# Performance work log

Measured on AMD Instinct MI355X. Metric: run time of the kernel, lower is better.

The kernel has to match this reference:

```python
import jax, jax.numpy as jnp
import numpy as np

N, E, D = 10000, 160000, 512


def setup_inputs() -> dict:
    key = jax.random.key(0)
    ks = jax.random.split(key, 5)
    x = jax.random.normal(ks[0], (N, D), dtype=jnp.float32)
    edge_index = jax.random.randint(ks[1], (2, E), 0, N, dtype=jnp.int32)
    W = jax.random.normal(ks[2], (D, D), dtype=jnp.float32) * (1.0 / np.sqrt(D))
    a_src = jax.random.normal(ks[3], (D,), dtype=jnp.float32) * 0.1
    a_dst = jax.random.normal(ks[4], (D,), dtype=jnp.float32) * 0.1
    bias = jnp.zeros((D,), dtype=jnp.float32)
    return {"x": x, "edge_index": edge_index, "W": W,
            "a_src": a_src, "a_dst": a_dst, "bias": bias}


def reference(x, edge_index, W, a_src, a_dst, bias):
    n = x.shape[0]
    # PyG GATConv default: add self-loops
    loops = jnp.arange(n, dtype=edge_index.dtype)
    src = jnp.concatenate([edge_index[0], loops])  # [E+N]
    dst = jnp.concatenate([edge_index[1], loops])  # [E+N]

    h = x @ W.T                                    # [N, D] linear projection
    e_src = h @ a_src                              # [N]
    e_dst = h @ a_dst                              # [N]
    e = e_src[src] + e_dst[dst]                    # [E+N]
    neg_slope = 0.2
    e = jnp.where(e > 0, e, neg_slope * e)         # leaky_relu

    # per-destination softmax (stable); self-loops guarantee non-empty segments
    m = jax.ops.segment_max(e, dst, num_segments=n)
    e = jnp.exp(e - m[dst])
    s = jax.ops.segment_sum(e, dst, num_segments=n)
    alpha = e / s[dst]                             # [E+N]

    msg = alpha[:, None] * h[src]                  # [E+N, D]
    out = jax.ops.segment_sum(msg, dst, num_segments=n) + bias  # [N, D]

    # module forward: x + elu(gat(x, edge_index))
    return x + jax.nn.elu(out)
```

## Files before the change

kernel.cpp:

```cpp
#include <hip/hip_runtime.h>
#include <hip/hip_bf16.h>

using bf16x8 = __attribute__((ext_vector_type(8))) __bf16;
using f32x4  = __attribute__((ext_vector_type(4))) float;

#define DFEAT 512
#define SLOTS 64

static __device__ __forceinline__ unsigned short f2bfbits(float f) {
    union { float f; unsigned int u; } v; v.f = f;
    unsigned int u = v.u;
    unsigned int r = (u + 0x7fffu + ((u >> 16) & 1u)) >> 16;
    return (unsigned short)r;
}

static __device__ __forceinline__ bf16x8 cvt8(float4 lo, float4 hi) {
    union { __hip_bfloat162 h2[4]; bf16x8 v; } u;
    u.h2[0] = __float22bfloat162_rn(make_float2(lo.x, lo.y));
    u.h2[1] = __float22bfloat162_rn(make_float2(lo.z, lo.w));
    u.h2[2] = __float22bfloat162_rn(make_float2(hi.x, hi.y));
    u.h2[3] = __float22bfloat162_rn(make_float2(hi.z, hi.w));
    return u.v;
}

__global__ __launch_bounds__(256, 2) void gemm_h_kernel(
    const float* __restrict__ X, const float* __restrict__ Wm,
    const int* __restrict__ srcv, const int* __restrict__ dstv,
    const float* __restrict__ avs, const float* __restrict__ avd,
    unsigned short* __restrict__ H, float* __restrict__ es, float* __restrict__ ed,
    int* __restrict__ cur, int* __restrict__ slot,
    int N, int E, int nBlocks)
{
    __shared__ unsigned short Bl[64 * 512];

    {
        int T = E + N;
        int stride = nBlocks * 256;
        for (int i = blockIdx.x * 256 + threadIdx.x; i < T; i += stride) {
            int s, d;
            if (i < E) { s = srcv[i]; d = dstv[i]; }
            else       { s = d = i - E; }
            int pos = atomicAdd(&cur[d], 1);
            if (pos < SLOTS) slot[(size_t)d * SLOTS + pos] = s;
        }
    }

    int L = blockIdx.x;
    int xcd = L & 7;
    int j   = L >> 3;
    int rpan = (j >> 3) * 8 + xcd;
    int cpan = j & 7;
    int rowPanels = (N + 127) >> 7;
    if (rpan >= rowPanels) return;
    int bm = rpan * 128;
    int bn = cpan * 64;

    int tid  = threadIdx.x;
    int wave = tid >> 6;
    int lane = tid & 63;
    int l15  = lane & 15;
    int quad = lane >> 4;

    for (int idx = tid; idx < 64 * 64; idx += 256) {
        int n = idx >> 6, c = idx & 63;
        const float4* wp = (const float4*)(Wm + (size_t)(bn + n) * DFEAT + c * 8);
        bf16x8 v = cvt8(wp[0], wp[1]);
        int cs = c ^ (n & 7);
        *(bf16x8*)((char*)Bl + (size_t)n * 1024 + cs * 16) = v;
    }
    __syncthreads();

    int r0 = bm + wave * 32 + l15;
    int r1 = r0 + 16;
    int ra0 = r0 < N ? r0 : N - 1;
    int ra1 = r1 < N ? r1 : N - 1;
    const float4* A0 = (const float4*)(X + (size_t)ra0 * DFEAT);
    const float4* A1 = (const float4*)(X + (size_t)ra1 * DFEAT);
    const char* Bc = (const char*)Bl;
    int xorm = l15 & 7;
    int roff0 = (0 * 16 + l15) * 1024;
    int roff1 = (1 * 16 + l15) * 1024;
    int roff2 = (2 * 16 + l15) * 1024;
    int roff3 = (3 * 16 + l15) * 1024;

    f32x4 acc[2][4] = {};

    float4 a0lo_c = A0[2 * quad],     a0hi_c = A0[2 * quad + 1];
    float4 a1lo_c = A1[2 * quad],     a1hi_c = A1[2 * quad + 1];
    int k1 = (4 + quad) * 2;
    float4 a0lo_n = A0[k1], a0hi_n = A0[k1 + 1];
    float4 a1lo_n = A1[k1], a1hi_n = A1[k1 + 1];
    bf16x8 b[4];
    {
        int cb = (quad ^ xorm) * 16;
        b[0] = *(const bf16x8*)(Bc + roff0 + cb);
        b[1] = *(const bf16x8*)(Bc + roff1 + cb);
        b[2] = *(const bf16x8*)(Bc + roff2 + cb);
        b[3] = *(const bf16x8*)(Bc + roff3 + cb);
    }

    for (int k0 = 0; k0 < 16; ++k0) {
        int ka = ((k0 + 2 < 16 ? k0 + 2 : 15) * 4 + quad) * 2;
        float4 f0lo = A0[ka], f0hi = A0[ka + 1];
        float4 f1lo = A1[ka], f1hi = A1[ka + 1];
        int kb = ((k0 + 1 < 16 ? k0 + 1 : 15) * 4) + quad;
        int cb = (kb ^ xorm) * 16;
        bf16x8 bn0 = *(const bf16x8*)(Bc + roff0 + cb);
        bf16x8 bn1 = *(const bf16x8*)(Bc + roff1 + cb);
        bf16x8 bn2 = *(const bf16x8*)(Bc + roff2 + cb);
        bf16x8 bn3 = *(const bf16x8*)(Bc + roff3 + cb);
        bf16x8 a0 = cvt8(a0lo_c, a0hi_c);
        bf16x8 a1 = cvt8(a1lo_c, a1hi_c);
        acc[0][0] = __builtin_amdgcn_mfma_f32_16x16x32_bf16(a0, b[0], acc[0][0], 0, 0, 0);
        acc[1][0] = __builtin_amdgcn_mfma_f32_16x16x32_bf16(a1, b[0], acc[1][0], 0, 0, 0);
        acc[0][1] = __builtin_amdgcn_mfma_f32_16x16x32_bf16(a0, b[1], acc[0][1], 0, 0, 0);
        acc[1][1] = __builtin_amdgcn_mfma_f32_16x16x32_bf16(a1, b[1], acc[1][1], 0, 0, 0);
        acc[0][2] = __builtin_amdgcn_mfma_f32_16x16x32_bf16(a0, b[2], acc[0][2], 0, 0, 0);
        acc[1][2] = __builtin_amdgcn_mfma_f32_16x16x32_bf16(a1, b[2], acc[1][2], 0, 0, 0);
        acc[0][3] = __builtin_amdgcn_mfma_f32_16x16x32_bf16(a0, b[3], acc[0][3], 0, 0, 0);
        acc[1][3] = __builtin_amdgcn_mfma_f32_16x16x32_bf16(a1, b[3], acc[1][3], 0, 0, 0);
        a0lo_c = a0lo_n; a0hi_c = a0hi_n; a1lo_c = a1lo_n; a1hi_c = a1hi_n;
        a0lo_n = f0lo;   a0hi_n = f0hi;   a1lo_n = f1lo;   a1hi_n = f1hi;
        b[0] = bn0; b[1] = bn1; b[2] = bn2; b[3] = bn3;
    }

    float as[4], ad[4];
    #pragma unroll
    for (int nt = 0; nt < 4; ++nt) {
        as[nt] = avs[bn + nt * 16 + l15];
        ad[nt] = avd[bn + nt * 16 + l15];
    }

    #pragma unroll
    for (int mt = 0; mt < 2; ++mt) {
        int rbase = bm + wave * 32 + mt * 16 + quad * 4;
        #pragma unroll
        for (int nt = 0; nt < 4; ++nt) {
            int col = bn + nt * 16 + l15;
            #pragma unroll
            for (int r = 0; r < 4; ++r) {
                int row = rbase + r;
                if (row < N) H[(size_t)row * DFEAT + col] = f2bfbits(acc[mt][nt][r]);
            }
        }
        #pragma unroll
        for (int r = 0; r < 4; ++r) {
            float ps = acc[mt][0][r] * as[0] + acc[mt][1][r] * as[1]
                     + acc[mt][2][r] * as[2] + acc[mt][3][r] * as[3];
            float pd = acc[mt][0][r] * ad[0] + acc[mt][1][r] * ad[1]
                     + acc[mt][2][r] * ad[2] + acc[mt][3][r] * ad[3];
            #pragma unroll
            for (int m = 1; m < 16; m <<= 1) {
                ps += __shfl_xor(ps, m);
                pd += __shfl_xor(pd, m);
            }
            int row = rbase + r;
            if (l15 == 0 && row < N) {
                atomicAdd(&es[row], ps);
                atomicAdd(&ed[row], pd);
            }
        }
    }
}

__global__ __launch_bounds__(256) void aggregate_kernel(
    const unsigned short* __restrict__ H, const float* __restrict__ x,
    const float* __restrict__ bias,
    const int* __restrict__ cur, const int* __restrict__ slot,
    const float* __restrict__ es, const float* __restrict__ ed,
    float* __restrict__ out, int N)
{
    int node = (blockIdx.x * 256 + threadIdx.x) >> 6;
    int lane = threadIdx.x & 63;
    if (node >= N) return;

    int k = cur[node];
    if (k > SLOTS) k = SLOTS;

    int   s = 0;
    float w = 0.f;
    if (lane < k) {
        s = slot[(size_t)node * SLOTS + lane];
        float e = es[s] + ed[node];
        e = e > 0.f ? e : 0.2f * e;
        w = __expf(e);
    }
    float denom = w;
    #pragma unroll
    for (int off = 32; off > 0; off >>= 1) denom += __shfl_xor(denom, off);
    float inv = 1.0f / denom;

    float a[8] = {};
    const unsigned short* Hl = H + lane * 8;

    auto fma8 = [&](uint4 hv, float wj) {
        a[0] += wj * __uint_as_float(hv.x << 16);
        a[1] += wj * __uint_as_float(hv.x & 0xffff0000u);
        a[2] += wj * __uint_as_float(hv.y << 16);
        a[3] += wj * __uint_as_float(hv.y & 0xffff0000u);
        a[4] += wj * __uint_as_float(hv.z << 16);
        a[5] += wj * __uint_as_float(hv.z & 0xffff0000u);
        a[6] += wj * __uint_as_float(hv.w << 16);
        a[7] += wj * __uint_as_float(hv.w & 0xffff0000u);
    };

    int j = 0;
    for (; j + 7 < k; j += 8) {
        uint4 h[8]; float wj[8];
        #pragma unroll
        for (int q = 0; q < 8; ++q) {
            int   sq = __shfl(s, j + q);
            wj[q]    = __shfl(w, j + q);
            h[q] = *(const uint4*)(Hl + (size_t)sq * DFEAT);
        }
        #pragma unroll
        for (int q = 0; q < 8; ++q) fma8(h[q], wj[q]);
    }
    if (j + 3 < k) {
        uint4 h[4]; float wj[4];
        #pragma unroll
        for (int q = 0; q < 4; ++q) {
            int   sq = __shfl(s, j + q);
            wj[q]    = __shfl(w, j + q);
            h[q] = *(const uint4*)(Hl + (size_t)sq * DFEAT);
        }
        #pragma unroll
        for (int q = 0; q < 4; ++q) fma8(h[q], wj[q]);
        j += 4;
    }
    for (; j < k; ++j) {
        int   sq = __shfl(s, j);
        float wj = __shfl(w, j);
        fma8(*(const uint4*)(Hl + (size_t)sq * DFEAT), wj);
    }

    int c = lane * 8;
    float4 b0 = *(const float4*)(bias + c);
    float4 b1 = *(const float4*)(bias + c + 4);
    float4 x0 = *(const float4*)(x + (size_t)node * DFEAT + c);
    float4 x1 = *(const float4*)(x + (size_t)node * DFEAT + c + 4);
    float r[8];
    r[0] = a[0] * inv + b0.x; r[1] = a[1] * inv + b0.y;
    r[2] = a[2] * inv + b0.z; r[3] = a[3] * inv + b0.w;
    r[4] = a[4] * inv + b1.x; r[5] = a[5] * inv + b1.y;
    r[6] = a[6] * inv + b1.z; r[7] = a[7] * inv + b1.w;
    #pragma unroll
    for (int i = 0; i < 8; ++i)
        r[i] = r[i] > 0.f ? r[i] : __expf(r[i]) - 1.f;
    float4 o0 = make_float4(x0.x + r[0], x0.y + r[1], x0.z + r[2], x0.w + r[3]);
    float4 o1 = make_float4(x1.x + r[4], x1.y + r[5], x1.z + r[6], x1.w + r[7]);
    *(float4*)(out + (size_t)node * DFEAT + c)     = o0;
    *(float4*)(out + (size_t)node * DFEAT + c + 4) = o1;
}

extern "C" void kernel_launch(void* const* d_in, const int* in_sizes, int n_in,
                              void* d_out, int out_size, void* d_ws, size_t ws_size,
                              hipStream_t stream)
{
    const float* x    = (const float*)d_in[0];
    const int*   edge = (const int*)d_in[1];
    const float* Wm   = (const float*)d_in[2];
    const float* avs  = (const float*)d_in[3];
    const float* avd  = (const float*)d_in[4];
    const float* bias = (const float*)d_in[5];

    const int D = DFEAT;
    const int N = in_sizes[0] / D;
    const int E = in_sizes[1] / 2;
    const int* srcv = edge;
    const int* dstv = edge + E;

    char* ws = (char*)d_ws;
    size_t off = 0;
    auto alloc = [&](size_t bytes) -> char* {
        char* p = ws + off;
        off += (bytes + 255) & ~(size_t)255;
        return p;
    };
    int*   cur  = (int*)alloc((size_t)N * 3 * 4);
    float* es   = (float*)(cur + N);
    float* ed   = es + N;
    int*   slot = (int*)alloc((size_t)N * SLOTS * 4);
    unsigned short* H = (unsigned short*)alloc((size_t)N * D * 2);

    hipMemsetAsync(cur, 0, (size_t)N * 3 * 4, stream);

    int rowPanels  = (N + 127) / 128;
    int rowPanels8 = ((rowPanels + 7) / 8) * 8;
    int nBlocks    = rowPanels8 * 8;
    gemm_h_kernel<<<dim3(nBlocks), 256, 0, stream>>>(
        x, Wm, srcv, dstv, avs, avd, H, es, ed, cur, slot, N, E, nBlocks);
    aggregate_kernel<<<dim3((N * 64 + 255) / 256), 256, 0, stream>>>(
        H, x, bias, cur, slot, es, ed, (float*)d_out, N);
}
```

Before: 150.8 us.

## Pre-convert W to bf16 in separate kernel, drop LDS staging, shrink GEMM tiles

```diff
diff --git a/kernel.cpp b/kernel.cpp
--- a/kernel.cpp
+++ b/kernel.cpp
@@ -23,105 +23,78 @@
     return u.v;
 }
 
-__global__ __launch_bounds__(256, 2) void gemm_h_kernel(
-    const float* __restrict__ X, const float* __restrict__ Wm,
+__global__ __launch_bounds__(256) void cvtw_scatter_kernel(
+    const float* __restrict__ w, unsigned short* __restrict__ Wb,
     const int* __restrict__ srcv, const int* __restrict__ dstv,
+    int* __restrict__ cur, int* __restrict__ slot,
+    int nw4, int E, int T)
+{
+    int i = blockIdx.x * 256 + threadIdx.x;
+    if (i < nw4) {
+        float4 v = ((const float4*)w)[i];
+        ushort4 u;
+        u.x = f2bfbits(v.x); u.y = f2bfbits(v.y);
+        u.z = f2bfbits(v.z); u.w = f2bfbits(v.w);
+        ((ushort4*)Wb)[i] = u;
+    }
+    if (i < T) {
+        int s, d;
+        if (i < E) { s = srcv[i]; d = dstv[i]; }
+        else       { s = d = i - E; }
+        int pos = atomicAdd(&cur[d], 1);
+        if (pos < SLOTS) slot[(size_t)d * SLOTS + pos] = s;
+    }
+}
+
+__global__ __launch_bounds__(256) void gemm_h_kernel(
+    const float* __restrict__ X, const unsigned short* __restrict__ Wb,
     const float* __restrict__ avs, const float* __restrict__ avd,
     unsigned short* __restrict__ H, float* __restrict__ es, float* __restrict__ ed,
-    int* __restrict__ cur, int* __restrict__ slot,
-    int N, int E, int nBlocks)
-{
-    __shared__ unsigned short Bl[64 * 512];
-
-    {
-        int T = E + N;
-        int stride = nBlocks * 256;
-        for (int i = blockIdx.x * 256 + threadIdx.x; i < T; i += stride) {
-            int s, d;
-            if (i < E) { s = srcv[i]; d = dstv[i]; }
-            else       { s = d = i - E; }
-            int pos = atomicAdd(&cur[d], 1);
-            if (pos < SLOTS) slot[(size_t)d * SLOTS + pos] = s;
-        }
-    }
-
-    int L = blockIdx.x;
-    int xcd = L & 7;
-    int j   = L >> 3;
-    int rpan = (j >> 3) * 8 + xcd;
-    int cpan = j & 7;
-    int rowPanels = (N + 127) >> 7;
+    int N, int rpanPad)
+{
+    int L    = blockIdx.x;
+    int rpan = L % rpanPad;
+    int cpan = L / rpanPad;
+    int rowPanels = (N + 63) >> 6;
     if (rpan >= rowPanels) return;
-    int bm = rpan * 128;
+    int bm = rpan * 64;
     int bn = cpan * 64;
 
-    int tid  = threadIdx.x;
-    int wave = tid >> 6;
-    int lane = tid & 63;
+    int wave = threadIdx.x >> 6;
+    int lane = threadIdx.x & 63;
     int l15  = lane & 15;
     int quad = lane >> 4;
 
-    for (int idx = tid; idx < 64 * 64; idx += 256) {
-        int n = idx >> 6, c = idx & 63;
-        const float4* wp = (const float4*)(Wm + (size_t)(bn + n) * DFEAT + c * 8);
-        bf16x8 v = cvt8(wp[0], wp[1]);
-        int cs = c ^ (n & 7);
-        *(bf16x8*)((char*)Bl + (size_t)n * 1024 + cs * 16) = v;
-    }
-    __syncthreads();
-
-    int r0 = bm + wave * 32 + l15;
-    int r1 = r0 + 16;
-    int ra0 = r0 < N ? r0 : N - 1;
-    int ra1 = r1 < N ? r1 : N - 1;
-    const float4* A0 = (const float4*)(X + (size_t)ra0 * DFEAT);
-    const float4* A1 = (const float4*)(X + (size_t)ra1 * DFEAT);
-    const char* Bc = (const char*)Bl;
-    int xorm = l15 & 7;
-    int roff0 = (0 * 16 + l15) * 1024;
-    int roff1 = (1 * 16 + l15) * 1024;
-    int roff2 = (2 * 16 + l15) * 1024;
-    int roff3 = (3 * 16 + l15) * 1024;
-
-    f32x4 acc[2][4] = {};
-
-    float4 a0lo_c = A0[2 * quad],     a0hi_c = A0[2 * quad + 1];
-    float4 a1lo_c = A1[2 * quad],     a1hi_c = A1[2 * quad + 1];
-    int k1 = (4 + quad) * 2;
-    float4 a0lo_n = A0[k1], a0hi_n = A0[k1 + 1];
-    float4 a1lo_n = A1[k1], a1hi_n = A1[k1 + 1];
-    bf16x8 b[4];
-    {
-        int cb = (quad ^ xorm) * 16;
-        b[0] = *(const bf16x8*)(Bc + roff0 + cb);
-        b[1] = *(const bf16x8*)(Bc + roff1 + cb);
-        b[2] = *(const bf16x8*)(Bc + roff2 + cb);
-        b[3] = *(const bf16x8*)(Bc + roff3 + cb);
-    }
+    int rowA = bm + wave * 16 + l15;
+    int ra   = rowA < N ? rowA : N - 1;
+
+    const float4* A = (const float4*)(X + (size_t)ra * DFEAT);
+    const bf16x8* B0 = (const bf16x8*)(Wb + (size_t)(bn +  0 + l15) * DFEAT);
+    const bf16x8* B1 = (const bf16x8*)(Wb + (size_t)(bn + 16 + l15) * DFEAT);
+    const bf16x8* B2 = (const bf16x8*)(Wb + (size_t)(bn + 32 + l15) * DFEAT);
+    const bf16x8* B3 = (const bf16x8*)(Wb + (size_t)(bn + 48 + l15) * DFEAT);
+
+    f32x4 acc[4] = {};
+
+    int k0i = quad * 2;
+    float4 alo_c = A[k0i], ahi_c = A[k0i + 1];
+    int k1i = (4 + quad) * 2;
+    float4 alo_n = A[k1i], ahi_n = A[k1i + 1];
+    bf16x8 b0c = B0[quad],     b1c = B1[quad],     b2c = B2[quad],     b3c = B3[quad];
+    bf16x8 b0n = B0[4 + quad], b1n = B1[4 + quad], b2n = B2[4 + quad], b3n = B3[4 + quad];
 
     for (int k0 = 0; k0 < 16; ++k0) {
-        int ka = ((k0 + 2 < 16 ? k0 + 2 : 15) * 4 + quad) * 2;
-        float4 f0lo = A0[ka], f0hi = A0[ka + 1];
-        float4 f1lo = A1[ka], f1hi = A1[ka + 1];
-        int kb = ((k0 + 1 < 16 ? k0 + 1 : 15) * 4) + quad;
-        int cb = (kb ^ xorm) * 16;
-        bf16x8 bn0 = *(const bf16x8*)(Bc + roff0 + cb);
-        bf16x8 bn1 = *(const bf16x8*)(Bc + roff1 + cb);
-        bf16x8 bn2 = *(const bf16x8*)(Bc + roff2 + cb);
-        bf16x8 bn3 = *(const bf16x8*)(Bc + roff3 + cb);
-        bf16x8 a0 = cvt8(a0lo_c, a0hi_c);
-        bf16x8 a1 = cvt8(a1lo_c, a1hi_c);
-        acc[0][0] = __builtin_amdgcn_mfma_f32_16x16x32_bf16(a0, b[0], acc[0][0], 0, 0, 0);
-        acc[1][0] = __builtin_amdgcn_mfma_f32_16x16x32_bf16(a1, b[0], acc[1][0], 0, 0, 0);
-        acc[0][1] = __builtin_amdgcn_mfma_f32_16x16x32_bf16(a0, b[1], acc[0][1], 0, 0, 0);
-        acc[1][1] = __builtin_amdgcn_mfma_f32_16x16x32_bf16(a1, b[1], acc[1][1], 0, 0, 0);
-        acc[0][2] = __builtin_amdgcn_mfma_f32_16x16x32_bf16(a0, b[2], acc[0][2], 0, 0, 0);
-        acc[1][2] = __builtin_amdgcn_mfma_f32_16x16x32_bf16(a1, b[2], acc[1][2], 0, 0, 0);
-        acc[0][3] = __builtin_amdgcn_mfma_f32_16x16x32_bf16(a0, b[3], acc[0][3], 0, 0, 0);
-        acc[1][3] = __builtin_amdgcn_mfma_f32_16x16x32_bf16(a1, b[3], acc[1][3], 0, 0, 0);
-        a0lo_c = a0lo_n; a0hi_c = a0hi_n; a1lo_c = a1lo_n; a1hi_c = a1hi_n;
-        a0lo_n = f0lo;   a0hi_n = f0hi;   a1lo_n = f1lo;   a1hi_n = f1hi;
-        b[0] = bn0; b[1] = bn1; b[2] = bn2; b[3] = bn3;
+        int kf = ((k0 + 2 < 16 ? k0 + 2 : 15) * 4) + quad;
+        float4 aflo = A[kf * 2], afhi = A[kf * 2 + 1];
+        bf16x8 b0f = B0[kf], b1f = B1[kf], b2f = B2[kf], b3f = B3[kf];
+        bf16x8 a = cvt8(alo_c, ahi_c);
+        acc[0] = __builtin_amdgcn_mfma_f32_16x16x32_bf16(a, b0c, acc[0], 0, 0, 0);
+        acc[1] = __builtin_amdgcn_mfma_f32_16x16x32_bf16(a, b1c, acc[1], 0, 0, 0);
+        acc[2] = __builtin_amdgcn_mfma_f32_16x16x32_bf16(a, b2c, acc[2], 0, 0, 0);
+        acc[3] = __builtin_amdgcn_mfma_f32_16x16x32_bf16(a, b3c, acc[3], 0, 0, 0);
+        alo_c = alo_n; ahi_c = ahi_n; alo_n = aflo; ahi_n = afhi;
+        b0c = b0n; b1c = b1n; b2c = b2n; b3c = b3n;
+        b0n = b0f; b1n = b1f; b2n = b2f; b3n = b3f;
     }
 
     float as[4], ad[4];
@@ -131,34 +104,31 @@
         ad[nt] = avd[bn + nt * 16 + l15];
     }
 
-    #pragma unroll
-    for (int mt = 0; mt < 2; ++mt) {
-        int rbase = bm + wave * 32 + mt * 16 + quad * 4;
-        #pragma unroll
-        for (int nt = 0; nt < 4; ++nt) {
-            int col = bn + nt * 16 + l15;
-            #pragma unroll
-            for (int r = 0; r < 4; ++r) {
-                int row = rbase + r;
-                if (row < N) H[(size_t)row * DFEAT + col] = f2bfbits(acc[mt][nt][r]);
-            }
-        }
+    int rbase = bm + wave * 16 + quad * 4;
+    #pragma unroll
+    for (int nt = 0; nt < 4; ++nt) {
+        int col = bn + nt * 16 + l15;
         #pragma unroll
         for (int r = 0; r < 4; ++r) {
-            float ps = acc[mt][0][r] * as[0] + acc[mt][1][r] * as[1]
-                     + acc[mt][2][r] * as[2] + acc[mt][3][r] * as[3];
-            float pd = acc[mt][0][r] * ad[0] + acc[mt][1][r] * ad[1]
-                     + acc[mt][2][r] * ad[2] + acc[mt][3][r] * ad[3];
-            #pragma unroll
-            for (int m = 1; m < 16; m <<= 1) {
-                ps += __shfl_xor(ps, m);
-                pd += __shfl_xor(pd, m);
-            }
             int row = rbase + r;
-            if (l15 == 0 && row < N) {
-                atomicAdd(&es[row], ps);
-                atomicAdd(&ed[row], pd);
-            }
+            if (row < N) H[(size_t)row * DFEAT + col] = f2bfbits(acc[nt][r]);
+        }
+    }
+    #pragma unroll
+    for (int r = 0; r < 4; ++r) {
+        float ps = acc[0][r] * as[0] + acc[1][r] * as[1]
+                 + acc[2][r] * as[2] + acc[3][r] * as[3];
+        float pd = acc[0][r] * ad[0] + acc[1][r] * ad[1]
+                 + acc[2][r] * ad[2] + acc[3][r] * ad[3];
+        #pragma unroll
+        for (int m = 1; m < 16; m <<= 1) {
+            ps += __shfl_xor(ps, m);
+            pd += __shfl_xor(pd, m);
+        }
+        int row = rbase + r;
+        if (l15 == 0 && row < N) {
+            atomicAdd(&es[row], ps);
+            atomicAdd(&ed[row], pd);
         }
     }
 }
@@ -267,6 +237,7 @@
     const int D = DFEAT;
     const int N = in_sizes[0] / D;
     const int E = in_sizes[1] / 2;
+    const int T = E + N;
     const int* srcv = edge;
     const int* dstv = edge + E;
 
@@ -281,15 +252,20 @@
     float* es   = (float*)(cur + N);
     float* ed   = es + N;
     int*   slot = (int*)alloc((size_t)N * SLOTS * 4);
-    unsigned short* H = (unsigned short*)alloc((size_t)N * D * 2);
+    unsigned short* Wb = (unsigned short*)alloc((size_t)D * D * 2);
+    unsigned short* H  = (unsigned short*)alloc((size_t)N * D * 2);
 
     hipMemsetAsync(cur, 0, (size_t)N * 3 * 4, stream);
 
-    int rowPanels  = (N + 127) / 128;
-    int rowPanels8 = ((rowPanels + 7) / 8) * 8;
-    int nBlocks    = rowPanels8 * 8;
-    gemm_h_kernel<<<dim3(nBlocks), 256, 0, stream>>>(
-        x, Wm, srcv, dstv, avs, avd, H, es, ed, cur, slot, N, E, nBlocks);
+    int nw4   = (D * D) / 4;
+    int grid0 = (nw4 > T ? nw4 : T);
+    cvtw_scatter_kernel<<<dim3((grid0 + 255) / 256), 256, 0, stream>>>(
+        Wm, Wb, srcv, dstv, cur, slot, nw4, E, T);
+
+    int rowPanels = (N + 63) / 64;
+    int rpanPad   = ((rowPanels + 7) / 8) * 8;
+    gemm_h_kernel<<<dim3(rpanPad * 8), 256, 0, stream>>>(
+        x, Wb, avs, avd, H, es, ed, N, rpanPad);
     aggregate_kernel<<<dim3((N * 64 + 255) / 256), 256, 0, stream>>>(
         H, x, bias, cur, slot, es, ed, (float*)d_out, N);
 }
```

Measured after the change: 178.3 us. +18.3%, slower.
